# Kernel optimization log

Hardware: AMD Instinct MI355X
Metric: run time of the kernel (lower is better)

The kernel has to match this reference:

```python
import jax, jax.numpy as jnp
import numpy as np
import math

N_KM = [64, 16]  # part_nums_hierarchical
SPATIAL = 891    # 11*9*9, hardcoded in the original reshape


def _make_im2cluster(C, K, seed):
    # random assignment but guarantee >=2 members per cluster (original code
    # indexes zs[0] and skips singleton clusters, but would crash on empties)
    rng = np.random.RandomState(seed)
    base = np.repeat(np.arange(K), 2)
    rest = rng.randint(0, K, size=C - base.size)
    return np.concatenate([base, rest]).astype(np.int64)


def setup_inputs() -> dict:
    key = jax.random.key(0)
    conv_features = jax.random.normal(key, (8, 4096, 11, 9, 9), dtype=jnp.float32)
    im2cluster_0 = jnp.asarray(_make_im2cluster(4096, 64, 1))
    im2cluster_1 = jnp.asarray(_make_im2cluster(4096, 16, 2))
    return {"conv_features": conv_features,
            "im2cluster_0": im2cluster_0,
            "im2cluster_1": im2cluster_1}


def _safe_norm(diff):
    # row-wise L2 norm, grad-safe at exactly-zero rows (row 0 is zs[0]-zs[0])
    sq = jnp.sum(diff * diff, axis=1)
    return jnp.where(sq > 0, jnp.sqrt(jnp.where(sq > 0, sq, 1.0)), 0.0)


def _hpro_loss(conv_features, im2clusters):
    bs, C = conv_features.shape[0], conv_features.shape[1]
    D = SPATIAL * bs
    x = conv_features.reshape(bs, C, SPATIAL)
    loss = jnp.float32(0.0)
    loss_node = jnp.float32(0.0)
    for m, K in enumerate(N_KM):
        im2c = np.asarray(im2clusters[m])  # constant indices -> concrete group sizes
        zs_m, conc_m = [], []
        for c in range(K):
            idx = np.nonzero(im2c == c)[0]
            # faithful torch reshape: [bs, n_c, 891] -> [n_c, 891*bs] (row-major)
            zs = x[:, idx, :].reshape(-1, D)
            n_c = zs.shape[0]
            norm_sum = jnp.sum(_safe_norm(zs - zs[0]))
            conc_m.append(norm_sum / (n_c * math.log(n_c + 10)))
            zs_m.append(zs)
        rs = jnp.stack([z[0] for z in zs_m], axis=1)  # [D, K] first-member reps
        for c in range(K):
            u1 = zs_m[c]
            if u1.shape[0] == 1:
                continue
            nom = jnp.sum(u1 * u1[0], axis=1) / conc_m[c]                     # [n_c]
            den = jax.scipy.special.logsumexp((u1 @ rs) / conc_m[c], axis=1)  # [n_c]
            loss = loss + (-(nom - den)).mean()
        if m == 0:
            loss_node = loss
    return loss_node / C, (loss - loss_node) / (len(N_KM) * C)


def reference(conv_features, im2cluster_0, im2cluster_1):
    return _hpro_loss(conv_features, [im2cluster_0, im2cluster_1])
```

## Files before the change

### kernel.cpp

```cpp
#include <hip/hip_runtime.h>
#include <math.h>

#define CCH 4096
#define SP 891
#define NSL 32768

typedef __attribute__((ext_vector_type(8))) short short8;
typedef __attribute__((ext_vector_type(4))) float f32x4;

__device__ __forceinline__ unsigned int pack_bf2(float a, float b) {
  unsigned int ua = __builtin_bit_cast(unsigned int, a);
  unsigned int ub = __builtin_bit_cast(unsigned int, b);
  ua = (ua + 0x7fffu + ((ua >> 16) & 1u)) >> 16;
  ub = (ub + 0x7fffu + ((ub >> 16) & 1u)) >> 16;
  return ua | (ub << 16);
}

__global__ void k_setup(const int* __restrict__ im0, const int* __restrict__ im1,
                        int* cnt0, int* off0, int* cnt1, int* off1,
                        int* mem0, int* mem1, int* rs0, int* rs1,
                        int* inv0, int* inv1) {
  int cb = blockIdx.x;
  int level = (cb >= 64) ? 1 : 0;
  int c = level ? cb - 64 : cb;
  const int* im = level ? im1 : im0;
  int* members = level ? mem1 : mem0;
  int* rs = level ? rs1 : rs0;
  int* inv = level ? inv1 : inv0;
  int lane = threadIdx.x;
  int lt = 0;
  for (int ch = lane; ch < CCH; ch += 64) lt += (im[ch] < c) ? 1 : 0;
  for (int o = 32; o; o >>= 1) lt += __shfl_xor(lt, o, 64);
  int base = lt;
  int cnt = 0;
  for (int chunk = 0; chunk < CCH; chunk += 64) {
    int ch = chunk + lane;
    bool m = (im[ch] == c);
    unsigned long long mk = __ballot(m);
    int pos = __popcll(mk & ((1ull << lane) - 1ull));
    if (m) members[base + cnt + pos] = ch;
    cnt += __popcll(mk);
  }
  int n = cnt;
  if (lane == 0) {
    if (level) { cnt1[c] = n; off1[c] = base; }
    else       { cnt0[c] = n; off0[c] = base; }
  }
  __syncthreads();
  for (int r = lane; r < n; r += 64) {
    #pragma unroll
    for (int q = 0; q < 8; q++) {
      int p = 8 * r + q;
      int b = p / n, j = p - b * n;
      int sid = b * CCH + members[base + j];
      rs[(size_t)(base + r) * 8 + q] = sid;
      inv[sid] = ((base + r) << 3) | q;
    }
  }
}

__global__ void k_brep(const float* __restrict__ X,
    const int* __restrict__ off0, const int* __restrict__ off1,
    const int* __restrict__ rs0, const int* __restrict__ rs1,
    uint4* __restrict__ Bfrag0, uint4* __restrict__ Bfrag1) {
  int gid = blockIdx.x * 4 + (threadIdx.x >> 6);
  int l = threadIdx.x & 63;
  int lrow = l & 15, hi = l >> 4;
  int level = (gid >= 32) ? 1 : 0;
  int q = level ? (gid - 32) : (gid >> 2);
  int ct = level ? 0 : (gid & 3);
  int cc = ct * 16 + lrow;
  int base = level ? off1[cc] : off0[cc];
  int sid = (level ? rs1 : rs0)[(size_t)base * 8 + q];
  const float* ap = X + (size_t)sid * SP + hi * 8;
  uint4* dst = (level ? Bfrag1 + (size_t)(q * 28) * 64
                      : Bfrag0 + (size_t)((q * 4 + ct) * 28) * 64) + l;
  #pragma unroll 3
  for (int kc = 0; kc < 27; kc++) {
    float4 fa0 = *(const float4*)(ap + kc * 32);
    float4 fa1 = *(const float4*)(ap + kc * 32 + 4);
    uint4 ua;
    ua.x = pack_bf2(fa0.x, fa0.y); ua.y = pack_bf2(fa0.z, fa0.w);
    ua.z = pack_bf2(fa1.x, fa1.y); ua.w = pack_bf2(fa1.z, fa1.w);
    dst[kc * 64] = ua;
  }
  {
    float4 fa0, fa1;
    if (hi == 3) {
      fa0 = make_float4(ap[864], ap[865], ap[866], 0.f);
      fa1 = make_float4(0.f, 0.f, 0.f, 0.f);
    } else {
      fa0 = *(const float4*)(ap + 864);
      fa1 = *(const float4*)(ap + 868);
    }
    uint4 ua;
    ua.x = pack_bf2(fa0.x, fa0.y); ua.y = pack_bf2(fa0.z, fa0.w);
    ua.z = pack_bf2(fa1.x, fa1.y); ua.w = pack_bf2(fa1.z, fa1.w);
    dst[27 * 64] = ua;
  }
}

__global__ __launch_bounds__(256) void k_pack2(const float* __restrict__ X,
    const int* __restrict__ inv0, const int* __restrict__ inv1,
    unsigned short* __restrict__ Y0, unsigned short* __restrict__ Y1,
    float* __restrict__ sn2) {
  const int w = threadIdx.x >> 6, l = threadIdx.x & 63;
  for (int sid = blockIdx.x * 4 + w; sid < NSL; sid += gridDim.x * 4) {
    const float* sp = X + (size_t)sid * SP;
    float4 v0, v1, v2, v3;
    {
      int el = 4 * l;
      v0 = *(const float4*)(sp + el);
      v1 = *(const float4*)(sp + 256 + el);
      v2 = *(const float4*)(sp + 512 + el);
      if (l <= 29)      v3 = *(const float4*)(sp + 768 + el);
      else if (l == 30) v3 = make_float4(sp[888], sp[889], sp[890], 0.f);
      else              v3 = make_float4(0.f, 0.f, 0.f, 0.f);
    }
    float s2 = v0.x * v0.x + v0.y * v0.y + v0.z * v0.z + v0.w * v0.w
             + v1.x * v1.x + v1.y * v1.y + v1.z * v1.z + v1.w * v1.w
             + v2.x * v2.x + v2.y * v2.y + v2.z * v2.z + v2.w * v2.w
             + v3.x * v3.x + v3.y * v3.y + v3.z * v3.z + v3.w * v3.w;
    for (int o = 32; o; o >>= 1) s2 += __shfl_xor(s2, o, 64);
    if (l == 0) sn2[sid] = s2;
    uint2 u0, u1, u2, u3;
    u0.x = pack_bf2(v0.x, v0.y); u0.y = pack_bf2(v0.z, v0.w);
    u1.x = pack_bf2(v1.x, v1.y); u1.y = pack_bf2(v1.z, v1.w);
    u2.x = pack_bf2(v2.x, v2.y); u2.y = pack_bf2(v2.z, v2.w);
    u3.x = pack_bf2(v3.x, v3.y); u3.y = pack_bf2(v3.z, v3.w);
    int i0 = inv0[sid], i1 = inv1[sid];
    unsigned short* d0 = Y0 + ((size_t)(i0 & 7) * CCH + (i0 >> 3)) * 896 + 4 * l;
    unsigned short* d1 = Y1 + ((size_t)(i1 & 7) * CCH + (i1 >> 3)) * 896 + 4 * l;
    *(uint2*)(d0) = u0;
    *(uint2*)(d0 + 256) = u1;
    *(uint2*)(d0 + 512) = u2;
    if (l < 32) *(uint2*)(d0 + 768) = u3;
    *(uint2*)(d1) = u0;
    *(uint2*)(d1 + 256) = u1;
    *(uint2*)(d1 + 512) = u2;
    if (l < 32) *(uint2*)(d1 + 768) = u3;
  }
}

__global__ __launch_bounds__(256) void k_gemm_all(
    const unsigned short* __restrict__ Y0, const unsigned short* __restrict__ Y1,
    const uint4* __restrict__ Bfrag0, const uint4* __restrict__ Bfrag1,
    float* __restrict__ P8_0, float* __restrict__ P8_1) {
  __shared__ __align__(16) unsigned short T[16 * 904];
  __shared__ float4 Rf[256];
  const int q = blockIdx.y, tid = threadIdx.x;
  const int lev = blockIdx.x >> 8;
  const int rt = blockIdx.x & 255;
  const int l = tid & 63, w = tid >> 6;
  const int lrow = l & 15, hi = l >> 4;
  const unsigned short* Y = lev ? Y1 : Y0;
  #pragma unroll
  for (int si = 0; si < 4; si++) {
    int i = w * 4 + si;
    const unsigned short* src = Y + ((size_t)q * CCH + rt * 16 + i) * 896;
    uint4 a0 = *(const uint4*)(src + l * 8);
    uint4 a1 = (l < 48) ? *(const uint4*)(src + 512 + l * 8) : make_uint4(0, 0, 0, 0);
    *(uint4*)(T + i * 904 + l * 8) = a0;
    if (l < 48) *(uint4*)(T + i * 904 + 512 + l * 8) = a1;
  }
  __syncthreads();
  const char* Abase = (const char*)T + lrow * 1808;
  if (!lev) {
    const uint4* bq = Bfrag0 + (size_t)((q * 4 + w) * 28) * 64 + l;
    f32x4 acc = {0.f, 0.f, 0.f, 0.f};
    short8 A0 = *(const short8*)(Abase + (0 * 64 + hi * 16));
    short8 A1 = *(const short8*)(Abase + (1 * 64 + hi * 16));
    uint4 B0 = bq[0 * 64], B1 = bq[1 * 64], B2 = bq[2 * 64], B3 = bq[3 * 64];
    #pragma unroll
    for (int kc = 0; kc < 28; kc++) {
      short8 a = (kc & 1) ? A1 : A0;
      uint4 b = (kc & 3) == 0 ? B0 : (kc & 3) == 1 ? B1 : (kc & 3) == 2 ? B2 : B3;
      acc = __builtin_amdgcn_mfma_f32_16x16x32_bf16(a, __builtin_bit_cast(short8, b), acc, 0, 0, 0);
      if (kc + 2 < 28) {
        short8 an = *(const short8*)(Abase + ((kc + 2) * 64 + hi * 16));
        if (kc & 1) A1 = an; else A0 = an;
      }
      if (kc + 4 < 28) {
        uint4 bn = bq[(kc + 4) * 64];
        switch (kc & 3) { case 0: B0 = bn; break; case 1: B1 = bn; break;
                          case 2: B2 = bn; break; default: B3 = bn; }
      }
    }
    #pragma unroll
    for (int r = 0; r < 4; r++) {
      int row = rt * 16 + hi * 4 + r;
      P8_0[((size_t)q * CCH + row) * 64 + w * 16 + lrow] = acc[r];
    }
  } else {
    const uint4* bq = Bfrag1 + (size_t)(q * 28) * 64 + l;
    f32x4 acc = {0.f, 0.f, 0.f, 0.f};
    #pragma unroll
    for (int kk = 0; kk < 7; kk++) {
      int kc = w * 7 + kk;
      short8 a = *(const short8*)(Abase + (kc * 64 + hi * 16));
      uint4 b = bq[kc * 64];
      acc = __builtin_amdgcn_mfma_f32_16x16x32_bf16(a, __builtin_bit_cast(short8, b), acc, 0, 0, 0);
    }
    __syncthreads();
    Rf[w * 64 + l] = make_float4(acc[0], acc[1], acc[2], acc[3]);
    __syncthreads();
    if (w == 0) {
      float4 v0 = Rf[l], v1 = Rf[64 + l], v2 = Rf[128 + l], v3 = Rf[192 + l];
      float vr[4] = { v0.x + v1.x + v2.x + v3.x, v0.y + v1.y + v2.y + v3.y,
                      v0.z + v1.z + v2.z + v3.z, v0.w + v1.w + v2.w + v3.w };
      #pragma unroll
      for (int r = 0; r < 4; r++) {
        int row = rt * 16 + hi * 4 + r;
        P8_1[((size_t)q * CCH + row) * 16 + lrow] = vr[r];
      }
    }
  }
}

template<int K>
__device__ __forceinline__ void fin_body(const float* __restrict__ P8,
    const float* __restrict__ sn2, const int* __restrict__ rs,
    const int* __restrict__ cnt, const int* __restrict__ off,
    double* __restrict__ clLoss, int c) {
  __shared__ float pcc[4096];
  __shared__ float red[512];
  __shared__ double redd[512];
  __shared__ float s_conc;
  const int n = cnt[c], base = off[c];
  const int tid = threadIdx.x;
  float rn0 = 0.f;
  #pragma unroll
  for (int qq = 0; qq < 8; qq++) rn0 += sn2[rs[(size_t)base * 8 + qq]];
  float t = 0.f;
  for (int r = tid; r < n; r += 512) {
    float pd = 0.f, rn = 0.f;
    #pragma unroll
    for (int qq = 0; qq < 8; qq++) {
      pd += P8[((size_t)qq * CCH + base + r) * K + c];
      rn += sn2[rs[(size_t)(base + r) * 8 + qq]];
    }
    pcc[r] = pd;
    if (r > 0) {
      float d2 = rn - 2.f * pd + rn0;
      t += (d2 > 0.f) ? sqrtf(d2) : 0.f;
    }
  }
  red[tid] = t; __syncthreads();
  for (int o = 256; o; o >>= 1) { if (tid < o) red[tid] += red[tid + o]; __syncthreads(); }
  if (tid == 0) s_conc = red[0] / ((float)n * logf((float)n + 10.f));
  __syncthreads();
  const float invc = 1.f / s_conc;
  const int wv = tid >> 6, lane = tid & 63;
  const int sub = (K == 64) ? 0 : (lane >> 4);
  const int cc = lane & (K - 1);
  constexpr int RPI = 8 * (64 / K);
  double acc = 0.0;
  for (int r = wv * (64 / K) + sub; r < n; r += RPI) {
    float s = 0.f;
    #pragma unroll
    for (int qq = 0; qq < 8; qq++) s += P8[((size_t)qq * CCH + base + r) * K + cc];
    float lg = s * invc;
    float m = lg;
    #pragma unroll
    for (int o = K / 2; o; o >>= 1) m = fmaxf(m, __shfl_xor(m, o, K));
    float e = expf(lg - m);
    float se = e;
    #pragma unroll
    for (int o = K / 2; o; o >>= 1) se += __shfl_xor(se, o, K);
    if (cc == 0) acc += (double)(m + logf(se)) - (double)(pcc[r] * invc);
  }
  redd[tid] = acc; __syncthreads();
  for (int o = 256; o; o >>= 1) { if (tid < o) redd[tid] += redd[tid + o]; __syncthreads(); }
  if (tid == 0) clLoss[c] = redd[0] / (double)n;
}

__global__ __launch_bounds__(512) void k_fin_all(const float* __restrict__ P8_0,
    const float* __restrict__ P8_1, const float* __restrict__ sn2,
    const int* __restrict__ rs0, const int* __restrict__ rs1,
    const int* __restrict__ cnt0, const int* __restrict__ off0,
    const int* __restrict__ cnt1, const int* __restrict__ off1,
    double* __restrict__ cl0, double* __restrict__ cl1) {
  if (blockIdx.x < 64) fin_body<64>(P8_0, sn2, rs0, cnt0, off0, cl0, blockIdx.x);
  else                 fin_body<16>(P8_1, sn2, rs1, cnt1, off1, cl1, blockIdx.x - 64);
}

__global__ void k_final(const double* __restrict__ cl0, const double* __restrict__ cl1,
                        float* __restrict__ out) {
  if (threadIdx.x == 0) {
    double s0 = 0.0, s1 = 0.0;
    for (int i = 0; i < 64; i++) s0 += cl0[i];
    for (int i = 0; i < 16; i++) s1 += cl1[i];
    out[0] = (float)(s0 / 4096.0);
    out[1] = (float)(s1 / 8192.0);
  }
}

extern "C" void kernel_launch(void* const* d_in, const int* in_sizes, int n_in,
                              void* d_out, int out_size, void* d_ws, size_t ws_size,
                              hipStream_t stream) {
  const float* X = (const float*)d_in[0];
  const int* im0 = (const int*)d_in[1];
  const int* im1 = (const int*)d_in[2];
  float* out = (float*)d_out;

  char* w = (char*)d_ws;
  auto alloc = [&](size_t bytes) -> char* {
    char* p = w; w += (bytes + 255) & ~(size_t)255; return p;
  };
  int*    cnt0  = (int*)alloc(64 * 4);
  int*    off0  = (int*)alloc(64 * 4);
  int*    cnt1  = (int*)alloc(16 * 4);
  int*    off1  = (int*)alloc(16 * 4);
  int*    mem0  = (int*)alloc((size_t)CCH * 4);
  int*    mem1  = (int*)alloc((size_t)CCH * 4);
  int*    rs0   = (int*)alloc((size_t)CCH * 8 * 4);
  int*    rs1   = (int*)alloc((size_t)CCH * 8 * 4);
  int*    inv0  = (int*)alloc((size_t)NSL * 4);
  int*    inv1  = (int*)alloc((size_t)NSL * 4);
  float*  sn2   = (float*)alloc((size_t)NSL * 4);
  uint4*  Bfrag0 = (uint4*)alloc((size_t)32 * 28 * 64 * 16);
  uint4*  Bfrag1 = (uint4*)alloc((size_t)8 * 28 * 64 * 16);
  unsigned short* Y0 = (unsigned short*)alloc((size_t)8 * CCH * 896 * 2);
  unsigned short* Y1 = (unsigned short*)alloc((size_t)8 * CCH * 896 * 2);
  float*  P8_0  = (float*)alloc((size_t)8 * CCH * 64 * 4);
  float*  P8_1  = (float*)alloc((size_t)8 * CCH * 16 * 4);
  double* cl0   = (double*)alloc(64 * 8);
  double* cl1   = (double*)alloc(16 * 8);

  k_setup<<<80, 64, 0, stream>>>(im0, im1, cnt0, off0, cnt1, off1,
                                 mem0, mem1, rs0, rs1, inv0, inv1);
  k_brep<<<10, 256, 0, stream>>>(X, off0, off1, rs0, rs1, Bfrag0, Bfrag1);
  k_pack2<<<2048, 256, 0, stream>>>(X, inv0, inv1, Y0, Y1, sn2);
  k_gemm_all<<<dim3(512, 8), 256, 0, stream>>>(Y0, Y1, Bfrag0, Bfrag1, P8_0, P8_1);
  k_fin_all<<<80, 512, 0, stream>>>(P8_0, P8_1, sn2, rs0, rs1, cnt0, off0, cnt1, off1, cl0, cl1);
  k_final<<<1, 64, 0, stream>>>(cl0, cl1, out);
}
```

Measured before the change: 123.5 us.

## Fuse bf16 packing into GEMM, computing all rep columns per slice in place

Removes the separate pack kernel and its permuted bf16 Y0/Y1 global buffers. Each block now loads 32 raw slices from X, converts them to bf16 in shared memory, and runs MFMA against every q-shifted representative fragment. Only the products whose q matches the slice's inverse index are written, into an output indexed by slice id. The finisher then gathers through rs indices. This saves a large global write and reread, but does 8x redundant MFMA work per slice and adds scattered gathers in the finisher.

```diff
diff --git a/kernel.cpp b/kernel.cpp
--- a/kernel.cpp
+++ b/kernel.cpp
@@ -100,125 +100,126 @@
   }
 }
 
-__global__ __launch_bounds__(256) void k_pack2(const float* __restrict__ X,
+template<int NC, int NT>
+__device__ __forceinline__ void run_group(
+    const unsigned short* T, const uint4* const* bp, const int* qv,
+    const int* s_inv, int sidBase, float* __restrict__ outP,
+    int ncol, int colbase, int l) {
+  const int lrow = l & 15, hi = l >> 4;
+  const char* Ab = (const char*)T + lrow * 1808;
+  f32x4 acc[NC][NT];
+  #pragma unroll
+  for (int c = 0; c < NC; c++)
+    #pragma unroll
+    for (int t = 0; t < NT; t++) acc[c][t] = (f32x4){0.f, 0.f, 0.f, 0.f};
+  uint4 B[NC][2];
+  #pragma unroll
+  for (int c = 0; c < NC; c++) { B[c][0] = bp[c][0]; B[c][1] = bp[c][64]; }
+  short8 A[NT][2];
+  #pragma unroll
+  for (int t = 0; t < NT; t++) {
+    A[t][0] = *(const short8*)(Ab + t * 16 * 1808 + 0 * 64 + hi * 16);
+    A[t][1] = *(const short8*)(Ab + t * 16 * 1808 + 1 * 64 + hi * 16);
+  }
+  #pragma unroll
+  for (int kc = 0; kc < 28; kc++) {
+    const int cur = kc & 1;
+    #pragma unroll
+    for (int c = 0; c < NC; c++)
+      #pragma unroll
+      for (int t = 0; t < NT; t++)
+        acc[c][t] = __builtin_amdgcn_mfma_f32_16x16x32_bf16(
+            A[t][cur], __builtin_bit_cast(short8, B[c][cur]), acc[c][t], 0, 0, 0);
+    if (kc + 2 < 28) {
+      #pragma unroll
+      for (int t = 0; t < NT; t++)
+        A[t][cur] = *(const short8*)(Ab + t * 16 * 1808 + (kc + 2) * 64 + hi * 16);
+      #pragma unroll
+      for (int c = 0; c < NC; c++) B[c][cur] = bp[c][(kc + 2) * 64];
+    }
+  }
+  #pragma unroll
+  for (int c = 0; c < NC; c++)
+    #pragma unroll
+    for (int t = 0; t < NT; t++)
+      #pragma unroll
+      for (int r = 0; r < 4; r++) {
+        int ls = t * 16 + hi * 4 + r;
+        if ((s_inv[ls] & 7) == qv[c])
+          outP[(size_t)(sidBase + ls) * ncol + colbase + lrow] = acc[c][t][r];
+      }
+}
+
+__global__ __launch_bounds__(256) void k_gemm_seq(const float* __restrict__ X,
     const int* __restrict__ inv0, const int* __restrict__ inv1,
-    unsigned short* __restrict__ Y0, unsigned short* __restrict__ Y1,
-    float* __restrict__ sn2) {
-  const int w = threadIdx.x >> 6, l = threadIdx.x & 63;
-  for (int sid = blockIdx.x * 4 + w; sid < NSL; sid += gridDim.x * 4) {
-    const float* sp = X + (size_t)sid * SP;
-    float4 v0, v1, v2, v3;
-    {
-      int el = 4 * l;
-      v0 = *(const float4*)(sp + el);
-      v1 = *(const float4*)(sp + 256 + el);
-      v2 = *(const float4*)(sp + 512 + el);
-      if (l <= 29)      v3 = *(const float4*)(sp + 768 + el);
-      else if (l == 30) v3 = make_float4(sp[888], sp[889], sp[890], 0.f);
-      else              v3 = make_float4(0.f, 0.f, 0.f, 0.f);
-    }
+    const uint4* __restrict__ Bfrag0, const uint4* __restrict__ Bfrag1,
+    float* __restrict__ P8a0, float* __restrict__ P8a1, float* __restrict__ sn2) {
+  __shared__ __align__(16) unsigned short T[32 * 904];
+  __shared__ int s_i0[32], s_i1[32];
+  const int tid = threadIdx.x;
+  const int l = tid & 63, w = tid >> 6;
+  const int sidBase = blockIdx.x * 32;
+  if (tid < 32) { s_i0[tid] = inv0[sidBase + tid]; s_i1[tid] = inv1[sidBase + tid]; }
+  for (int si = w; si < 32; si += 4) {
+    const float* sp = X + (size_t)(sidBase + si) * SP;
+    float4 v0 = *(const float4*)(sp + 4 * l);
+    float4 v1 = *(const float4*)(sp + 256 + 4 * l);
+    float4 v2 = *(const float4*)(sp + 512 + 4 * l);
+    float4 v3;
+    if (l <= 29)      v3 = *(const float4*)(sp + 768 + 4 * l);
+    else if (l == 30) v3 = make_float4(sp[888], sp[889], sp[890], 0.f);
+    else              v3 = make_float4(0.f, 0.f, 0.f, 0.f);
     float s2 = v0.x * v0.x + v0.y * v0.y + v0.z * v0.z + v0.w * v0.w
              + v1.x * v1.x + v1.y * v1.y + v1.z * v1.z + v1.w * v1.w
              + v2.x * v2.x + v2.y * v2.y + v2.z * v2.z + v2.w * v2.w
              + v3.x * v3.x + v3.y * v3.y + v3.z * v3.z + v3.w * v3.w;
     for (int o = 32; o; o >>= 1) s2 += __shfl_xor(s2, o, 64);
-    if (l == 0) sn2[sid] = s2;
-    uint2 u0, u1, u2, u3;
-    u0.x = pack_bf2(v0.x, v0.y); u0.y = pack_bf2(v0.z, v0.w);
-    u1.x = pack_bf2(v1.x, v1.y); u1.y = pack_bf2(v1.z, v1.w);
-    u2.x = pack_bf2(v2.x, v2.y); u2.y = pack_bf2(v2.z, v2.w);
-    u3.x = pack_bf2(v3.x, v3.y); u3.y = pack_bf2(v3.z, v3.w);
-    int i0 = inv0[sid], i1 = inv1[sid];
-    unsigned short* d0 = Y0 + ((size_t)(i0 & 7) * CCH + (i0 >> 3)) * 896 + 4 * l;
-    unsigned short* d1 = Y1 + ((size_t)(i1 & 7) * CCH + (i1 >> 3)) * 896 + 4 * l;
-    *(uint2*)(d0) = u0;
-    *(uint2*)(d0 + 256) = u1;
-    *(uint2*)(d0 + 512) = u2;
-    if (l < 32) *(uint2*)(d0 + 768) = u3;
-    *(uint2*)(d1) = u0;
-    *(uint2*)(d1 + 256) = u1;
-    *(uint2*)(d1 + 512) = u2;
-    if (l < 32) *(uint2*)(d1 + 768) = u3;
-  }
-}
-
-__global__ __launch_bounds__(256) void k_gemm_all(
-    const unsigned short* __restrict__ Y0, const unsigned short* __restrict__ Y1,
-    const uint4* __restrict__ Bfrag0, const uint4* __restrict__ Bfrag1,
-    float* __restrict__ P8_0, float* __restrict__ P8_1) {
-  __shared__ __align__(16) unsigned short T[16 * 904];
-  __shared__ float4 Rf[256];
-  const int q = blockIdx.y, tid = threadIdx.x;
-  const int lev = blockIdx.x >> 8;
-  const int rt = blockIdx.x & 255;
-  const int l = tid & 63, w = tid >> 6;
-  const int lrow = l & 15, hi = l >> 4;
-  const unsigned short* Y = lev ? Y1 : Y0;
-  #pragma unroll
-  for (int si = 0; si < 4; si++) {
-    int i = w * 4 + si;
-    const unsigned short* src = Y + ((size_t)q * CCH + rt * 16 + i) * 896;
-    uint4 a0 = *(const uint4*)(src + l * 8);
-    uint4 a1 = (l < 48) ? *(const uint4*)(src + 512 + l * 8) : make_uint4(0, 0, 0, 0);
-    *(uint4*)(T + i * 904 + l * 8) = a0;
-    if (l < 48) *(uint4*)(T + i * 904 + 512 + l * 8) = a1;
+    if (l == 0) sn2[sidBase + si] = s2;
+    unsigned short* Tr = T + si * 904;
+    uint2 u;
+    u.x = pack_bf2(v0.x, v0.y); u.y = pack_bf2(v0.z, v0.w);
+    *(uint2*)(Tr + 4 * l) = u;
+    u.x = pack_bf2(v1.x, v1.y); u.y = pack_bf2(v1.z, v1.w);
+    *(uint2*)(Tr + 256 + 4 * l) = u;
+    u.x = pack_bf2(v2.x, v2.y); u.y = pack_bf2(v2.z, v2.w);
+    *(uint2*)(Tr + 512 + 4 * l) = u;
+    if (l < 32) {
+      u.x = pack_bf2(v3.x, v3.y); u.y = pack_bf2(v3.z, v3.w);
+      *(uint2*)(Tr + 768 + 4 * l) = u;
+    }
   }
   __syncthreads();
-  const char* Abase = (const char*)T + lrow * 1808;
-  if (!lev) {
-    const uint4* bq = Bfrag0 + (size_t)((q * 4 + w) * 28) * 64 + l;
-    f32x4 acc = {0.f, 0.f, 0.f, 0.f};
-    short8 A0 = *(const short8*)(Abase + (0 * 64 + hi * 16));
-    short8 A1 = *(const short8*)(Abase + (1 * 64 + hi * 16));
-    uint4 B0 = bq[0 * 64], B1 = bq[1 * 64], B2 = bq[2 * 64], B3 = bq[3 * 64];
-    #pragma unroll
-    for (int kc = 0; kc < 28; kc++) {
-      short8 a = (kc & 1) ? A1 : A0;
-      uint4 b = (kc & 3) == 0 ? B0 : (kc & 3) == 1 ? B1 : (kc & 3) == 2 ? B2 : B3;
-      acc = __builtin_amdgcn_mfma_f32_16x16x32_bf16(a, __builtin_bit_cast(short8, b), acc, 0, 0, 0);
-      if (kc + 2 < 28) {
-        short8 an = *(const short8*)(Abase + ((kc + 2) * 64 + hi * 16));
-        if (kc & 1) A1 = an; else A0 = an;
-      }
-      if (kc + 4 < 28) {
-        uint4 bn = bq[(kc + 4) * 64];
-        switch (kc & 3) { case 0: B0 = bn; break; case 1: B1 = bn; break;
-                          case 2: B2 = bn; break; default: B3 = bn; }
-      }
-    }
-    #pragma unroll
-    for (int r = 0; r < 4; r++) {
-      int row = rt * 16 + hi * 4 + r;
-      P8_0[((size_t)q * CCH + row) * 64 + w * 16 + lrow] = acc[r];
-    }
-  } else {
-    const uint4* bq = Bfrag1 + (size_t)(q * 28) * 64 + l;
-    f32x4 acc = {0.f, 0.f, 0.f, 0.f};
-    #pragma unroll
-    for (int kk = 0; kk < 7; kk++) {
-      int kc = w * 7 + kk;
-      short8 a = *(const short8*)(Abase + (kc * 64 + hi * 16));
-      uint4 b = bq[kc * 64];
-      acc = __builtin_amdgcn_mfma_f32_16x16x32_bf16(a, __builtin_bit_cast(short8, b), acc, 0, 0, 0);
-    }
-    __syncthreads();
-    Rf[w * 64 + l] = make_float4(acc[0], acc[1], acc[2], acc[3]);
-    __syncthreads();
-    if (w == 0) {
-      float4 v0 = Rf[l], v1 = Rf[64 + l], v2 = Rf[128 + l], v3 = Rf[192 + l];
-      float vr[4] = { v0.x + v1.x + v2.x + v3.x, v0.y + v1.y + v2.y + v3.y,
-                      v0.z + v1.z + v2.z + v3.z, v0.w + v1.w + v2.w + v3.w };
-      #pragma unroll
-      for (int r = 0; r < 4; r++) {
-        int row = rt * 16 + hi * 4 + r;
-        P8_1[((size_t)q * CCH + row) * 16 + lrow] = vr[r];
-      }
-    }
+  {
+    const uint4* bp[4]; int qv[4];
+    #pragma unroll
+    for (int c = 0; c < 4; c++) {
+      bp[c] = Bfrag0 + (size_t)((c * 4 + w) * 28) * 64 + l;
+      qv[c] = c;
+    }
+    run_group<4, 2>(T, bp, qv, s_i0, sidBase, P8a0, 64, w * 16, l);
+  }
+  {
+    const uint4* bp[4]; int qv[4];
+    #pragma unroll
+    for (int c = 0; c < 4; c++) {
+      bp[c] = Bfrag0 + (size_t)(((4 + c) * 4 + w) * 28) * 64 + l;
+      qv[c] = 4 + c;
+    }
+    run_group<4, 2>(T, bp, qv, s_i0, sidBase, P8a0, 64, w * 16, l);
+  }
+  {
+    const uint4* bp[2]; int qv[2];
+    #pragma unroll
+    for (int c = 0; c < 2; c++) {
+      bp[c] = Bfrag1 + (size_t)((2 * w + c) * 28) * 64 + l;
+      qv[c] = 2 * w + c;
+    }
+    run_group<2, 2>(T, bp, qv, s_i1, sidBase, P8a1, 16, 0, l);
   }
 }
 
 template<int K>
-__device__ __forceinline__ void fin_body(const float* __restrict__ P8,
+__device__ __forceinline__ void fin_body(const float* __restrict__ P8a,
     const float* __restrict__ sn2, const int* __restrict__ rs,
     const int* __restrict__ cnt, const int* __restrict__ off,
     double* __restrict__ clLoss, int c) {
@@ -236,8 +237,9 @@
     float pd = 0.f, rn = 0.f;
     #pragma unroll
     for (int qq = 0; qq < 8; qq++) {
-      pd += P8[((size_t)qq * CCH + base + r) * K + c];
-      rn += sn2[rs[(size_t)(base + r) * 8 + qq]];
+      int sid = rs[(size_t)(base + r) * 8 + qq];
+      pd += P8a[(size_t)sid * K + c];
+      rn += sn2[sid];
     }
     pcc[r] = pd;
     if (r > 0) {
@@ -258,7 +260,8 @@
   for (int r = wv * (64 / K) + sub; r < n; r += RPI) {
     float s = 0.f;
     #pragma unroll
-    for (int qq = 0; qq < 8; qq++) s += P8[((size_t)qq * CCH + base + r) * K + cc];
+    for (int qq = 0; qq < 8; qq++)
+      s += P8a[(size_t)rs[(size_t)(base + r) * 8 + qq] * K + cc];
     float lg = s * invc;
     float m = lg;
     #pragma unroll
@@ -274,14 +277,14 @@
   if (tid == 0) clLoss[c] = redd[0] / (double)n;
 }
 
-__global__ __launch_bounds__(512) void k_fin_all(const float* __restrict__ P8_0,
-    const float* __restrict__ P8_1, const float* __restrict__ sn2,
+__global__ __launch_bounds__(512) void k_fin_all(const float* __restrict__ P8a0,
+    const float* __restrict__ P8a1, const float* __restrict__ sn2,
     const int* __restrict__ rs0, const int* __restrict__ rs1,
     const int* __restrict__ cnt0, const int* __restrict__ off0,
     const int* __restrict__ cnt1, const int* __restrict__ off1,
     double* __restrict__ cl0, double* __restrict__ cl1) {
-  if (blockIdx.x < 64) fin_body<64>(P8_0, sn2, rs0, cnt0, off0, cl0, blockIdx.x);
-  else                 fin_body<16>(P8_1, sn2, rs1, cnt1, off1, cl1, blockIdx.x - 64);
+  if (blockIdx.x < 64) fin_body<64>(P8a0, sn2, rs0, cnt0, off0, cl0, blockIdx.x);
+  else                 fin_body<16>(P8a1, sn2, rs1, cnt1, off1, cl1, blockIdx.x - 64);
 }
 
 __global__ void k_final(const double* __restrict__ cl0, const double* __restrict__ cl1,
@@ -320,18 +323,17 @@
   float*  sn2   = (float*)alloc((size_t)NSL * 4);
   uint4*  Bfrag0 = (uint4*)alloc((size_t)32 * 28 * 64 * 16);
   uint4*  Bfrag1 = (uint4*)alloc((size_t)8 * 28 * 64 * 16);
-  unsigned short* Y0 = (unsigned short*)alloc((size_t)8 * CCH * 896 * 2);
-  unsigned short* Y1 = (unsigned short*)alloc((size_t)8 * CCH * 896 * 2);
-  float*  P8_0  = (float*)alloc((size_t)8 * CCH * 64 * 4);
-  float*  P8_1  = (float*)alloc((size_t)8 * CCH * 16 * 4);
+  float*  P8a0  = (float*)alloc((size_t)NSL * 64 * 4);
+  float*  P8a1  = (float*)alloc((size_t)NSL * 16 * 4);
   double* cl0   = (double*)alloc(64 * 8);
   double* cl1   = (double*)alloc(16 * 8);
 
   k_setup<<<80, 64, 0, stream>>>(im0, im1, cnt0, off0, cnt1, off1,
                                  mem0, mem1, rs0, rs1, inv0, inv1);
   k_brep<<<10, 256, 0, stream>>>(X, off0, off1, rs0, rs1, Bfrag0, Bfrag1);
-  k_pack2<<<2048, 256, 0, stream>>>(X, inv0, inv1, Y0, Y1, sn2);
-  k_gemm_all<<<dim3(512, 8), 256, 0, stream>>>(Y0, Y1, Bfrag0, Bfrag1, P8_0, P8_1);
-  k_fin_all<<<80, 512, 0, stream>>>(P8_0, P8_1, sn2, rs0, rs1, cnt0, off0, cnt1, off1, cl0, cl1);
+  k_gemm_seq<<<NSL / 32, 256, 0, stream>>>(X, inv0, inv1, Bfrag0, Bfrag1,
+                                           P8a0, P8a1, sn2);
+  k_fin_all<<<80, 512, 0, stream>>>(P8a0, P8a1, sn2, rs0, rs1,
+                                    cnt0, off0, cnt1, off1, cl0, cl1);
   k_final<<<1, 64, 0, stream>>>(cl0, cl1, out);
 }
```

Result: slower. 360.9 us (+192.2%).
